# Performance work log

Hardware: AMD Instinct MI355X
Metric: run time of the kernel (lower is better)

Reference implementation:

```python
import jax, jax.numpy as jnp
import numpy as np

S_DIM = 256   # summary_dim
L_DIM = 64    # latent_dim
H = 128       # hidden_dim
NL = 2        # num_layers
BATCH = 512
SEQ_LEN = 1024


def setup_inputs() -> dict:
    key = jax.random.key(0)
    ks = jax.random.split(key, 20)
    w = lambda k, shape, s=0.08: (jax.random.normal(k, shape, jnp.float32) * s)
    in0 = L_DIM + S_DIM  # LSTM layer-0 input size (cat of prev output + summary)
    return {
        "z_summary": jax.random.normal(ks[0], (BATCH, S_DIM), jnp.float32),
        "seq_len": SEQ_LEN,
        # summary -> initial hidden/cell states (Linear)
        "W_init_h": w(ks[1], (H * NL, S_DIM)),
        "b_init_h": w(ks[2], (H * NL,)),
        "W_init_c": w(ks[3], (H * NL, S_DIM)),
        "b_init_c": w(ks[4], (H * NL,)),
        # LSTM layer 0 (PyTorch gate order: i, f, g, o)
        "W_ih0": w(ks[5], (4 * H, in0)),
        "W_hh0": w(ks[6], (4 * H, H)),
        "b_ih0": w(ks[7], (4 * H,)),
        "b_hh0": w(ks[8], (4 * H,)),
        # LSTM layer 1
        "W_ih1": w(ks[9], (4 * H, H)),
        "W_hh1": w(ks[10], (4 * H, H)),
        "b_ih1": w(ks[11], (4 * H,)),
        "b_hh1": w(ks[12], (4 * H,)),
        # output head: Linear(H, L_DIM) + Tanh
        "W_out": w(ks[13], (L_DIM, H)),
        "b_out": w(ks[14], (L_DIM,)),
    }


def _lstm_cell(x, h, c, W_ih, W_hh, b_ih, b_hh):
    gates = x @ W_ih.T + b_ih + h @ W_hh.T + b_hh
    i, f, g, o = jnp.split(gates, 4, axis=-1)  # PyTorch gate order
    c_new = jax.nn.sigmoid(f) * c + jax.nn.sigmoid(i) * jnp.tanh(g)
    h_new = jax.nn.sigmoid(o) * jnp.tanh(c_new)
    return h_new, c_new


def reference(z_summary, seq_len, W_init_h, b_init_h, W_init_c, b_init_c,
              W_ih0, W_hh0, b_ih0, b_hh0, W_ih1, W_hh1, b_ih1, b_hh1,
              W_out, b_out):
    B = z_summary.shape[0]
    # init_hidden/init_cell: (B, NL*H) -> per-layer states (B, H)
    h0 = (z_summary @ W_init_h.T + b_init_h).reshape(B, NL, H)
    c0 = (z_summary @ W_init_c.T + b_init_c).reshape(B, NL, H)
    h_prev0 = jnp.zeros((B, L_DIM), z_summary.dtype)
    carry0 = (h0[:, 0], c0[:, 0], h0[:, 1], c0[:, 1], h_prev0)

    def step(carry, _):
        h_l0, c_l0, h_l1, c_l1, h_prev = carry
        x = jnp.concatenate([h_prev, z_summary], axis=-1)  # (B, L_DIM+S_DIM)
        h_l0, c_l0 = _lstm_cell(x, h_l0, c_l0, W_ih0, W_hh0, b_ih0, b_hh0)
        # dropout between layers is inference-mode identity
        h_l1, c_l1 = _lstm_cell(h_l0, h_l1, c_l1, W_ih1, W_hh1, b_ih1, b_hh1)
        h_t = jnp.tanh(h_l1 @ W_out.T + b_out)  # output head, fed back
        return (h_l0, c_l0, h_l1, c_l1, h_t), h_t

    _, ys = jax.lax.scan(step, carry0, None, length=seq_len)  # (T, B, L_DIM)
    return jnp.transpose(ys, (1, 0, 2))  # (B, T, L_DIM)
```

## Files before the change

kernel.cpp:

```cpp
#include <hip/hip_runtime.h>


#define DI __device__ __forceinline__

typedef float f32x4 __attribute__((ext_vector_type(4)));
typedef _Float16 h16x4 __attribute__((ext_vector_type(4)));
typedef _Float16 h16x8 __attribute__((ext_vector_type(8)));

DI f32x4 mm(h16x8 a, h16x8 b, f32x4 c) {
  return __builtin_amdgcn_mfma_f32_16x16x32_f16(a, b, c, 0, 0, 0);
}

DI float sigm_(float x) {
  float e = __expf(-x);
  return __builtin_amdgcn_rcpf(1.0f + e);
}
DI float tanh_(float x) {
  float e = __expf(-2.0f * x);
  return __builtin_fmaf(2.0f, __builtin_amdgcn_rcpf(1.0f + e), -1.0f);
}
DI h16x8 cvt8h(const float* __restrict__ p) {
  f32x4 a = *(const f32x4*)p;
  f32x4 b = *(const f32x4*)(p + 4);
  _Float16 t[8];
#pragma unroll
  for (int i = 0; i < 4; ++i) {
    t[i]     = (_Float16)a[i];
    t[4 + i] = (_Float16)b[i];
  }
  return *(h16x8*)t;
}

#define L_H0 0
#define L_H1 12800
#define L_WO 21504
#define L_AZ 37888
#define L_OB 46336
#define L_WL 48384
#define L_TOT 146688
static_assert(L_TOT <= 163840, "LDS budget (160 KiB/CU)");

template <int P>
DI void lstm_step(unsigned char* smem,
                  const h16x8 (&wf0)[20], const h16x8 (&wf1)[24],
                  f32x4 (&acc)[4], float& c0r, float& c1r,
                  h16x4 xzr, f32x4 bvr, float bo,
                  int a0off, int a1off, int v16, int wlb,
                  int w0off, int w1off, int oboff, int obro,
                  int wv, int t, float* outp0) {
  constexpr int h0r = L_H0 + P * 6400, h0w = L_H0 + 6400 - P * 6400;
  constexpr int h1r = L_H1 + P * 4352, h1w = L_H1 + 4352 - P * 4352;

  f32x4 acc2[4];
  {
    h16x8 af4 = *(const h16x8*)(smem + h0r + a0off + 4 * 64);
    h16x8 af5 = *(const h16x8*)(smem + h0r + a0off + 5 * 64);
#pragma unroll
    for (int g = 0; g < 4; ++g)
      acc[g] = mm(af4, wf0[16 + g], acc[g]);
#pragma unroll
    for (int g = 0; g < 4; ++g) {
      h16x8 bf = *(const h16x8*)(smem + wlb + g * 1024);
      acc[g] = mm(af5, bf, acc[g]);
    }
  }
#pragma unroll
  for (int g = 0; g < 4; ++g) {
    f32x4 a = {bvr[g], bvr[g], bvr[g], bvr[g]};
    acc2[g] = a;
  }
#pragma unroll
  for (int kc = 4; kc < 8; ++kc) {
    h16x8 af = *(const h16x8*)(smem + h1r + a1off + (kc - 4) * 64);
#pragma unroll
    for (int g = 0; g < 4; ++g) {
      h16x8 bf = (kc < 6)
          ? wf1[kc * 4 + g]
          : *(const h16x8*)(smem + wlb + ((kc - 6) * 4 + g + 4) * 1024);
      acc2[g] = mm(af, bf, acc2[g]);
    }
  }
  {
    float ig = sigm_(acc[0][0]), fg = sigm_(acc[1][0]);
    float gg = tanh_(acc[2][0]), og = sigm_(acc[3][0]);
    c0r = fg * c0r + ig * gg;
    *(_Float16*)(smem + h0w + w0off) = (_Float16)(og * tanh_(c0r));
  }
  __syncthreads();

#pragma unroll
  for (int kc = 0; kc < 4; ++kc) {
    h16x8 af = *(const h16x8*)(smem + h0w + a0off + kc * 64);
#pragma unroll
    for (int g = 0; g < 4; ++g)
      acc2[g] = mm(af, wf1[kc * 4 + g], acc2[g]);
  }
  {
    float ig = sigm_(acc2[0][0]), fg = sigm_(acc2[1][0]);
    float gg = tanh_(acc2[2][0]), og = sigm_(acc2[3][0]);
    c1r = fg * c1r + ig * gg;
    *(_Float16*)(smem + h1w + w1off) = (_Float16)(og * tanh_(c1r));
  }
  __syncthreads();

  if (wv < 4) {
    f32x4 ao = {bo, bo, bo, bo};
#pragma unroll
    for (int kc = 0; kc < 4; ++kc) {
      h16x8 af  = *(const h16x8*)(smem + h1w + a1off + kc * 64);
      h16x8 bfr = *(const h16x8*)(smem + L_WO + kc * 4096 + v16);
      ao = mm(af, bfr, ao);
    }
    float v = tanh_(ao[0]);
    *(float*)(smem + L_OB + P * 1024 + oboff) = v;
    *(_Float16*)(smem + h0w + w0off + 256) = (_Float16)v;
  }
#pragma unroll
  for (int g = 0; g < 4; ++g) {
    float v = (float)xzr[g];
    f32x4 a = {v, v, v, v};
    acc[g] = a;
  }
#pragma unroll
  for (int kc = 0; kc < 4; ++kc) {
    h16x8 af = *(const h16x8*)(smem + h0w + a0off + kc * 64);
#pragma unroll
    for (int g = 0; g < 4; ++g)
      acc[g] = mm(af, wf0[kc * 4 + g], acc[g]);
  }
  __syncthreads();

  if (P) {
    float vv = *(const float*)(smem + L_OB + obro);
    *(outp0 + (unsigned)(t - 1) * 64u) = vv;
  }
}

__global__ __launch_bounds__(512, 2) void k_main(
    const float* __restrict__ z,
    const float* __restrict__ W_init_h, const float* __restrict__ b_init_h,
    const float* __restrict__ W_init_c, const float* __restrict__ b_init_c,
    const float* __restrict__ W_ih0, const float* __restrict__ W_hh0,
    const float* __restrict__ b_ih0, const float* __restrict__ b_hh0,
    const float* __restrict__ W_ih1, const float* __restrict__ W_hh1,
    const float* __restrict__ b_ih1, const float* __restrict__ b_hh1,
    const float* __restrict__ W_out, const float* __restrict__ b_out,
    float* __restrict__ out) {
  __shared__ __align__(16) unsigned char smem[L_TOT];
  const int tid = threadIdx.x;
  const int w = tid >> 6, l = tid & 63;
  const int l15 = l & 15, l4 = l >> 4;
  const int bl = blockIdx.x, b0i = bl << 2;
  const int col = 16 * w + l15;

  {
    int zm = tid >> 5, zk = (tid & 31) * 8;
    h16x8 zv;
    if ((zm & 3) == 0) {
      zv = cvt8h(z + (b0i + (zm >> 2)) * 256 + zk);
    } else {
      _Float16 t[8] = {};
      zv = *(h16x8*)t;
    }
    *(h16x8*)(smem + L_AZ + zm * 528 + zk * 2) = zv;
    for (int i = tid; i < 1024; i += 512) {
      int li = i & 63, f = i >> 6;
      int kc = f >> 2, wv = f & 3;
      int n = 16 * wv + (li & 15), k0 = kc * 32 + ((li >> 4) & 3) * 8;
      *(h16x8*)(smem + L_WO + i * 16) = cvt8h(W_out + n * 128 + k0);
    }
#pragma unroll
    for (int f = 0; f < 12; ++f) {
      int g = f & 3;
      int n = g * 128 + col;
      const float* src;
      if (f < 4) {
        src = W_ih0 + n * 320 + (32 + l4 * 8);
      } else {
        int kc = 6 + ((f - 4) >> 2);
        src = W_hh1 + n * 128 + (kc * 32 + l4 * 8 - 128);
      }
      *(h16x8*)(smem + L_WL + ((w * 12 + f) * 64 + l) * 16) = cvt8h(src);
    }
    if (tid < 256) {
      int r2 = tid >> 4, c2 = (tid & 15) * 4;
      h16x4 zz = {(_Float16)0, (_Float16)0, (_Float16)0, (_Float16)0};
      *(h16x4*)(smem + L_H0 + r2 * 400 + 256 + c2 * 2) = zz;
    }
  }
  f32x4 bvr;
#pragma unroll
  for (int g = 0; g < 4; ++g)
    bvr[g] = b_ih1[g * 128 + col] + b_hh1[g * 128 + col];
  float bo = (w < 4) ? b_out[col] : 0.0f;
  __syncthreads();

  float c0i, c1i;
  h16x4 xzr;
  {
    f32x4 xza[4], ha[2], ca[2];
#pragma unroll
    for (int g = 0; g < 4; ++g) {
      float b = b_ih0[g * 128 + col] + b_hh0[g * 128 + col];
      f32x4 a = {b, b, b, b}; xza[g] = a;
    }
#pragma unroll
    for (int layer = 0; layer < 2; ++layer) {
      float bh = b_init_h[layer * 128 + col];
      float bc = b_init_c[layer * 128 + col];
      f32x4 ah = {bh, bh, bh, bh}; ha[layer] = ah;
      f32x4 ac = {bc, bc, bc, bc}; ca[layer] = ac;
    }
#pragma unroll
    for (int kc = 0; kc < 8; ++kc) {
      h16x8 az = *(const h16x8*)(smem + L_AZ + l15 * 528 + kc * 64 + l4 * 16);
      int kofs = kc * 32 + l4 * 8;
#pragma unroll
      for (int g = 0; g < 4; ++g) {
        h16x8 bz = cvt8h(W_ih0 + (g * 128 + col) * 320 + 64 + kofs);
        xza[g] = mm(az, bz, xza[g]);
      }
#pragma unroll
      for (int layer = 0; layer < 2; ++layer) {
        h16x8 bh = cvt8h(W_init_h + (layer * 128 + col) * 256 + kofs);
        ha[layer] = mm(az, bh, ha[layer]);
        h16x8 bc = cvt8h(W_init_c + (layer * 128 + col) * 256 + kofs);
        ca[layer] = mm(az, bc, ca[layer]);
      }
    }
#pragma unroll
    for (int r = 0; r < 4; ++r) {
      int m = l4 * 4 + r;
      *(_Float16*)(smem + L_H0 + m * 400 + col * 2) = (_Float16)ha[0][r];
      *(_Float16*)(smem + L_H1 + m * 272 + col * 2) = (_Float16)ha[1][r];
    }
    c0i = ca[0][0]; c1i = ca[1][0];
    _Float16 t[4];
#pragma unroll
    for (int g = 0; g < 4; ++g) t[g] = (_Float16)xza[g][0];
    xzr = *(h16x4*)t;
  }

  h16x8 wf0[20], wf1[24];
#pragma unroll
  for (int kc = 0; kc < 5; ++kc)
#pragma unroll
    for (int g = 0; g < 4; ++g) {
      int n = g * 128 + col, k0 = kc * 32 + l4 * 8;
      const float* src = (k0 < 128) ? (W_hh0 + n * 128 + k0)
                                    : (W_ih0 + n * 320 + (k0 - 128));
      wf0[kc * 4 + g] = cvt8h(src);
    }
#pragma unroll
  for (int kc = 0; kc < 6; ++kc)
#pragma unroll
    for (int g = 0; g < 4; ++g) {
      int n = g * 128 + col, k0 = kc * 32 + l4 * 8;
      const float* src = (k0 < 128) ? (W_ih1 + n * 128 + k0)
                                    : (W_hh1 + n * 128 + (k0 - 128));
      wf1[kc * 4 + g] = cvt8h(src);
    }

  float c0r = c0i, c1r = c1i;

  const int a0off = (l15 & 12) * 400 + l4 * 16;
  const int a1off = (l15 & 12) * 272 + l4 * 16;
  const int v16   = tid * 16;
  const int wlb   = L_WL + (w * 12 * 64 + l) * 16;
  const int w0off = (4 * l4) * 400 + col * 2;
  const int w1off = (4 * l4) * 272 + col * 2;
  const int oboff = l4 * 256 + col * 4;
  const int obro  = (tid >> 8) * 1024 + ((tid >> 6) & 3) * 256 + (tid & 63) * 4;
  float* outp0 = out + (unsigned long long)(b0i + ((tid >> 6) & 3)) * 65536ull +
                 (tid >> 8) * 64 + (tid & 63);
  __syncthreads();

  f32x4 acc[4];
#pragma unroll
  for (int g = 0; g < 4; ++g) {
    float v = (float)xzr[g];
    f32x4 a = {v, v, v, v};
    acc[g] = a;
  }
#pragma unroll
  for (int kc = 0; kc < 4; ++kc) {
    h16x8 af = *(const h16x8*)(smem + L_H0 + a0off + kc * 64);
#pragma unroll
    for (int g = 0; g < 4; ++g)
      acc[g] = mm(af, wf0[kc * 4 + g], acc[g]);
  }

  for (int t2 = 0; t2 < 1024; t2 += 2) {
    lstm_step<0>(smem, wf0, wf1, acc, c0r, c1r, xzr, bvr, bo, a0off, a1off,
                 v16, wlb, w0off, w1off, oboff, obro, w, t2, outp0);
    lstm_step<1>(smem, wf0, wf1, acc, c0r, c1r, xzr, bvr, bo, a0off, a1off,
                 v16, wlb, w0off, w1off, oboff, obro, w, t2 + 1, outp0);
  }
}

extern "C" void kernel_launch(void* const* d_in, const int* in_sizes, int n_in,
                              void* d_out, int out_size, void* d_ws, size_t ws_size,
                              hipStream_t stream) {
  (void)in_sizes; (void)n_in; (void)out_size; (void)d_ws; (void)ws_size;
  const float* z        = (const float*)d_in[0];
  const float* W_init_h = (const float*)d_in[2];
  const float* b_init_h = (const float*)d_in[3];
  const float* W_init_c = (const float*)d_in[4];
  const float* b_init_c = (const float*)d_in[5];
  const float* W_ih0 = (const float*)d_in[6];
  const float* W_hh0 = (const float*)d_in[7];
  const float* b_ih0 = (const float*)d_in[8];
  const float* b_hh0 = (const float*)d_in[9];
  const float* W_ih1 = (const float*)d_in[10];
  const float* W_hh1 = (const float*)d_in[11];
  const float* b_ih1 = (const float*)d_in[12];
  const float* b_hh1 = (const float*)d_in[13];
  const float* W_out = (const float*)d_in[14];
  const float* b_out = (const float*)d_in[15];
  float* out = (float*)d_out;

  k_main<<<dim3(128), dim3(512), 0, stream>>>(
      z, W_init_h, b_init_h, W_init_c, b_init_c,
      W_ih0, W_hh0, b_ih0, b_hh0, W_ih1, W_hh1, b_ih1, b_hh1,
      W_out, b_out, out);
}
```

Measured before the change: 2.062 ms.

## Defer layer-1 recurrent MFMAs after barrier and run output head on all waves

```diff
diff --git a/kernel.cpp b/kernel.cpp
--- a/kernel.cpp
+++ b/kernel.cpp
@@ -45,13 +45,12 @@
                   const h16x8 (&wf0)[20], const h16x8 (&wf1)[24],
                   f32x4 (&acc)[4], float& c0r, float& c1r,
                   h16x4 xzr, f32x4 bvr, float bo,
-                  int a0off, int a1off, int v16, int wlb,
+                  int a0off, int a1off, int wo_off, int wlb,
                   int w0off, int w1off, int oboff, int obro,
                   int wv, int t, float* outp0) {
   constexpr int h0r = L_H0 + P * 6400, h0w = L_H0 + 6400 - P * 6400;
   constexpr int h1r = L_H1 + P * 4352, h1w = L_H1 + 4352 - P * 4352;
 
-  f32x4 acc2[4];
   {
     h16x8 af4 = *(const h16x8*)(smem + h0r + a0off + 4 * 64);
     h16x8 af5 = *(const h16x8*)(smem + h0r + a0off + 5 * 64);
@@ -62,22 +61,6 @@
     for (int g = 0; g < 4; ++g) {
       h16x8 bf = *(const h16x8*)(smem + wlb + g * 1024);
       acc[g] = mm(af5, bf, acc[g]);
-    }
-  }
-#pragma unroll
-  for (int g = 0; g < 4; ++g) {
-    f32x4 a = {bvr[g], bvr[g], bvr[g], bvr[g]};
-    acc2[g] = a;
-  }
-#pragma unroll
-  for (int kc = 4; kc < 8; ++kc) {
-    h16x8 af = *(const h16x8*)(smem + h1r + a1off + (kc - 4) * 64);
-#pragma unroll
-    for (int g = 0; g < 4; ++g) {
-      h16x8 bf = (kc < 6)
-          ? wf1[kc * 4 + g]
-          : *(const h16x8*)(smem + wlb + ((kc - 6) * 4 + g + 4) * 1024);
-      acc2[g] = mm(af, bf, acc2[g]);
     }
   }
   {
@@ -89,31 +72,37 @@
   __syncthreads();
 
 #pragma unroll
-  for (int kc = 0; kc < 4; ++kc) {
-    h16x8 af = *(const h16x8*)(smem + h0w + a0off + kc * 64);
-#pragma unroll
-    for (int g = 0; g < 4; ++g)
-      acc2[g] = mm(af, wf1[kc * 4 + g], acc2[g]);
-  }
-  {
-    float ig = sigm_(acc2[0][0]), fg = sigm_(acc2[1][0]);
-    float gg = tanh_(acc2[2][0]), og = sigm_(acc2[3][0]);
+  for (int g = 0; g < 4; ++g) {
+    f32x4 a = {bvr[g], bvr[g], bvr[g], bvr[g]};
+    acc[g] = a;
+  }
+#pragma unroll
+  for (int kc = 0; kc < 8; ++kc) {
+    h16x8 af = (kc < 4)
+        ? *(const h16x8*)(smem + h0w + a0off + kc * 64)
+        : *(const h16x8*)(smem + h1r + a1off + (kc - 4) * 64);
+#pragma unroll
+    for (int g = 0; g < 4; ++g) {
+      h16x8 bf = (kc < 6)
+          ? wf1[kc * 4 + g]
+          : *(const h16x8*)(smem + wlb + ((kc - 6) * 4 + g + 4) * 1024);
+      acc[g] = mm(af, bf, acc[g]);
+    }
+  }
+  {
+    float ig = sigm_(acc[0][0]), fg = sigm_(acc[1][0]);
+    float gg = tanh_(acc[2][0]), og = sigm_(acc[3][0]);
     c1r = fg * c1r + ig * gg;
     *(_Float16*)(smem + h1w + w1off) = (_Float16)(og * tanh_(c1r));
   }
   __syncthreads();
 
-  if (wv < 4) {
-    f32x4 ao = {bo, bo, bo, bo};
-#pragma unroll
-    for (int kc = 0; kc < 4; ++kc) {
-      h16x8 af  = *(const h16x8*)(smem + h1w + a1off + kc * 64);
-      h16x8 bfr = *(const h16x8*)(smem + L_WO + kc * 4096 + v16);
-      ao = mm(af, bfr, ao);
-    }
-    float v = tanh_(ao[0]);
-    *(float*)(smem + L_OB + P * 1024 + oboff) = v;
-    *(_Float16*)(smem + h0w + w0off + 256) = (_Float16)v;
+  f32x4 ao = {bo, bo, bo, bo};
+#pragma unroll
+  for (int kc = 0; kc < 4; ++kc) {
+    h16x8 af  = *(const h16x8*)(smem + h1w + a1off + kc * 64);
+    h16x8 bfr = *(const h16x8*)(smem + L_WO + kc * 4096 + wo_off);
+    ao = mm(af, bfr, ao);
   }
 #pragma unroll
   for (int g = 0; g < 4; ++g) {
@@ -127,6 +116,11 @@
 #pragma unroll
     for (int g = 0; g < 4; ++g)
       acc[g] = mm(af, wf0[kc * 4 + g], acc[g]);
+  }
+  if (wv < 4) {
+    float v = tanh_(ao[0]);
+    *(float*)(smem + L_OB + P * 1024 + oboff) = v;
+    *(_Float16*)(smem + h0w + w0off + 256) = (_Float16)v;
   }
   __syncthreads();
 
@@ -192,7 +186,7 @@
 #pragma unroll
   for (int g = 0; g < 4; ++g)
     bvr[g] = b_ih1[g * 128 + col] + b_hh1[g * 128 + col];
-  float bo = (w < 4) ? b_out[col] : 0.0f;
+  float bo = b_out[16 * (w & 3) + l15];
   __syncthreads();
 
   float c0i, c1i;
@@ -265,7 +259,7 @@
 
   const int a0off = (l15 & 12) * 400 + l4 * 16;
   const int a1off = (l15 & 12) * 272 + l4 * 16;
-  const int v16   = tid * 16;
+  const int wo_off = ((w & 3) * 64 + l) * 16;
   const int wlb   = L_WL + (w * 12 * 64 + l) * 16;
   const int w0off = (4 * l4) * 400 + col * 2;
   const int w1off = (4 * l4) * 272 + col * 2;
@@ -292,9 +286,9 @@
 
   for (int t2 = 0; t2 < 1024; t2 += 2) {
     lstm_step<0>(smem, wf0, wf1, acc, c0r, c1r, xzr, bvr, bo, a0off, a1off,
-                 v16, wlb, w0off, w1off, oboff, obro, w, t2, outp0);
+                 wo_off, wlb, w0off, w1off, oboff, obro, w, t2, outp0);
     lstm_step<1>(smem, wf0, wf1, acc, c0r, c1r, xzr, bvr, bo, a0off, a1off,
-                 v16, wlb, w0off, w1off, oboff, obro, w, t2 + 1, outp0);
+                 wo_off, wlb, w0off, w1off, oboff, obro, w, t2 + 1, outp0);
   }
 }
 
```

New measurement: 2.079 ms. Within noise of the previous version (+0.8%).
